# Performance work log

Hardware: AMD Instinct MI355X
Metric: run time of the kernel (lower is better)

The kernel has to match this reference:

```python
import jax, jax.numpy as jnp
import numpy as np

N, E, D = 100_000, 1_250_000, 64
EPS = 1e-8

def setup_inputs() -> dict:
    key = jax.random.key(0)
    ks = jax.random.split(key, 8)
    h = jax.random.normal(ks[0], (N, D), jnp.float32)
    eig = jax.random.normal(ks[1], (E, 1), jnp.float32)          # per-edge vector field
    snorm_n = jax.random.uniform(ks[2], (N, 1), jnp.float32)     # node norm
    src = jax.random.randint(ks[3], (E,), 0, N)
    dst = jax.random.randint(ks[4], (E,), 0, N)
    # pretrans: Linear(2D -> D); posttrans: Linear((3+1)*D -> D); torch Linear weight is [out, in]
    W1 = jax.random.normal(ks[5], (D, 2 * D), jnp.float32) / np.sqrt(2.0 * D)
    b1 = jnp.zeros((D,), jnp.float32)
    W2 = jax.random.normal(ks[6], (D, 4 * D), jnp.float32) / np.sqrt(4.0 * D)
    b2 = jnp.zeros((D,), jnp.float32)
    gamma = jnp.ones((D,), jnp.float32)   # BatchNorm1d weight
    beta = jnp.zeros((D,), jnp.float32)   # BatchNorm1d bias
    return dict(h=h, eig=eig, snorm_n=snorm_n, src=src, dst=dst,
                W1=W1, b1=b1, W2=W2, b2=b2, gamma=gamma, beta=beta)

def reference(h, eig, snorm_n, src, dst, W1, b1, W2, b2, gamma, beta):
    seg = lambda x: jax.ops.segment_sum(x, dst, num_segments=N)
    # pretrans on edges: MLP(cat[h_src, h_dst])
    z2 = jnp.concatenate([h[src], h[dst]], axis=1)   # [E, 2D]
    e = z2 @ W1.T + b1                                # [E, D]
    deg = seg(jnp.ones((E, 1), e.dtype))              # [N, 1]
    # aggregator: mean
    agg_mean = seg(e) / jnp.maximum(deg, 1.0)
    # aggregator: max (empty segments -> 0)
    agg_max = jax.ops.segment_max(e, dst, num_segments=N)
    agg_max = jnp.where(deg > 0, agg_max, 0.0)
    # aggregator: directional derivative dir_dx
    absum = seg(jnp.abs(eig))                         # [N, 1] sum of |vf| per node
    w = eig / (absum[dst] + EPS)                      # [E, 1] normalized weights
    agg_dir = jnp.abs(seg(e * w) - seg(w) * h)        # [N, D]
    # posttrans on nodes
    hc = jnp.concatenate([h, agg_mean, agg_max, agg_dir], axis=1)  # [N, 4D]
    h2 = (hc @ W2.T + b2) * snorm_n
    # BatchNorm1d (training mode: batch stats, biased variance)
    mu = jnp.mean(h2, axis=0)
    var = jnp.var(h2, axis=0)
    h2 = (h2 - mu) * jax.lax.rsqrt(var + 1e-5) * gamma + beta
    h2 = jax.nn.relu(h2)
    # residual (in_dim == out_dim); dropout p=0 is identity
    return h + h2
```

## Files before the change

kernel.cpp:

```cpp
#include <hip/hip_runtime.h>
#include <math.h>

__device__ __forceinline__ float bf2f(unsigned short s) {
    return __uint_as_float(((unsigned)s) << 16);
}
__device__ __forceinline__ unsigned short f2bf(float f) {
    unsigned u = __float_as_uint(f);
    unsigned r = (u + 0x7fffu + ((u >> 16) & 1u)) >> 16;
    return (unsigned short)r;
}

__global__ __launch_bounds__(256) void edge_rank_kernel(
    const int* __restrict__ dst, int* __restrict__ cursor, int* __restrict__ rank, int E)
{
    int e = blockIdx.x * 256 + threadIdx.x;
    if (e < E) {
        rank[e] = atomicAdd(&cursor[dst[e]], 1);
    }
}

__global__ __launch_bounds__(256) void block_reduce_kernel(
    const int* __restrict__ deg, int* __restrict__ bsum, int N)
{
    __shared__ int sd[256];
    int t = threadIdx.x;
    int i = blockIdx.x * 256 + t;
    sd[t] = (i < N) ? deg[i] : 0;
    __syncthreads();
    for (int s = 128; s > 0; s >>= 1) {
        if (t < s) sd[t] += sd[t + s];
        __syncthreads();
    }
    if (t == 0) bsum[blockIdx.x] = sd[0];
}

__global__ __launch_bounds__(1024) void scan_bsums_kernel(
    const int* __restrict__ bsum, int* __restrict__ bscan, int nb)
{
    __shared__ int sd[1024];
    int t = threadIdx.x;
    int own = (t < nb) ? bsum[t] : 0;
    sd[t] = own;
    __syncthreads();
    for (int off = 1; off < 1024; off <<= 1) {
        int v = (t >= off) ? sd[t - off] : 0;
        __syncthreads();
        sd[t] += v;
        __syncthreads();
    }
    if (t < nb) bscan[t] = sd[t] - own;
}

__global__ __launch_bounds__(256) void block_scan_kernel(
    const int* __restrict__ deg, const int* __restrict__ bscan,
    int* __restrict__ offs, int N)
{
    __shared__ int sd[256];
    int t = threadIdx.x;
    int i = blockIdx.x * 256 + t;
    int myv = (i < N) ? deg[i] : 0;
    sd[t] = myv;
    __syncthreads();
    for (int off = 1; off < 256; off <<= 1) {
        int v = (t >= off) ? sd[t - off] : 0;
        __syncthreads();
        sd[t] += v;
        __syncthreads();
    }
    if (i < N) {
        offs[i] = sd[t] - myv + bscan[blockIdx.x];
    }
}

__global__ __launch_bounds__(256) void csr_scatter_kernel(
    const int* __restrict__ src, const int* __restrict__ dst, const float* __restrict__ eig,
    const int* __restrict__ rank, const int* __restrict__ offs,
    int2* __restrict__ csr, int E)
{
    int e = blockIdx.x * 256 + threadIdx.x;
    if (e < E) {
        int dn = dst[e];
        int p = offs[dn] + rank[e];
        csr[p] = make_int2(src[e], __float_as_int(eig[e]));
    }
}

__global__ __launch_bounds__(256) void uv_kernel(
    const float* __restrict__ h, const float* __restrict__ W1, const float* __restrict__ b1,
    unsigned short* __restrict__ u, unsigned short* __restrict__ v, int N)
{
    __shared__ float wT[64 * 128];
    __shared__ float hs[64 * 68];
    int t = threadIdx.x;
    for (int idx = t; idx < 64 * 128; idx += 256) {
        int j = idx >> 7, c = idx & 127;
        int d = c & 63;
        int col = (c < 64) ? j : (64 + j);
        wT[idx] = W1[d * 128 + col];
    }
    int n0 = blockIdx.x * 64;
    for (int r = 0; r < 16; ++r) {
        int idx = r * 256 + t;
        int nl = idx >> 6, j = idx & 63;
        int n = n0 + nl;
        hs[nl * 68 + j] = (n < N) ? h[(size_t)n * 64 + j] : 0.f;
    }
    __syncthreads();

    int nb = (t & 15) * 4;
    int cb = (t >> 4) * 8;
    float acc[4][8];
#pragma unroll
    for (int i = 0; i < 4; ++i)
#pragma unroll
        for (int k = 0; k < 8; ++k) acc[i][k] = 0.f;

    for (int j = 0; j < 64; ++j) {
        float wv[8];
#pragma unroll
        for (int k = 0; k < 8; ++k) wv[k] = wT[j * 128 + cb + k];
#pragma unroll
        for (int i = 0; i < 4; ++i) {
            float hv = hs[(nb + i) * 68 + j];
#pragma unroll
            for (int k = 0; k < 8; ++k) acc[i][k] = fmaf(hv, wv[k], acc[i][k]);
        }
    }

    bool isV = (cb >= 64);
    int dbase = cb & 63;
#pragma unroll
    for (int i = 0; i < 4; ++i) {
        int n = n0 + nb + i;
        if (n < N) {
            union { unsigned short s[8]; uint4 v4; } pk;
            if (!isV) {
#pragma unroll
                for (int k = 0; k < 8; ++k) pk.s[k] = f2bf(acc[i][k]);
                *(uint4*)(u + (size_t)n * 64 + dbase) = pk.v4;
            } else {
#pragma unroll
                for (int k = 0; k < 8; ++k) pk.s[k] = f2bf(acc[i][k] + b1[dbase + k]);
                *(uint4*)(v + (size_t)n * 64 + dbase) = pk.v4;
            }
        }
    }
}

__global__ __launch_bounds__(256) void w2t_kernel(
    const float* __restrict__ W2, float* __restrict__ w2t)
{
    int idx = blockIdx.x * 256 + threadIdx.x;
    if (idx < 64 * 256) {
        int d = idx >> 8, k = idx & 255;
        w2t[k * 64 + d] = W2[idx];
    }
}

__global__ __launch_bounds__(256) void agg_kernel(
    const unsigned short* __restrict__ u, const unsigned short* __restrict__ v,
    const float* __restrict__ h,
    const int* __restrict__ offs, const int* __restrict__ degi,
    const int2* __restrict__ csr,
    unsigned short* __restrict__ agg, int N)
{
    int gw = (blockIdx.x * 256 + threadIdx.x) >> 6;
    int lane = threadIdx.x & 63;
    int n = __builtin_amdgcn_readfirstlane(gw);
    if (n >= N) return;
    int beg = offs[n];
    int dn = degi[n];

    float accs = 0.f, accd = 0.f, accm = -3.402823466e38f;
    float pa = 0.f, ps = 0.f;
    for (int i0 = 0; i0 < dn; i0 += 64) {
        int cnt = min(dn - i0, 64);
        int idxv = 0; float wvv = 0.f;
        if (lane < cnt) {
            int2 rec = csr[beg + i0 + lane];
            idxv = rec.x;
            wvv = __int_as_float(rec.y);
        }
        pa += fabsf(wvv);
        ps += wvv;
        int j = 0;
        for (; j + 4 <= cnt; j += 4) {
            int s0 = __shfl(idxv, j), s1 = __shfl(idxv, j + 1);
            int s2 = __shfl(idxv, j + 2), s3 = __shfl(idxv, j + 3);
            float w0 = __shfl(wvv, j), w1 = __shfl(wvv, j + 1);
            float w2_ = __shfl(wvv, j + 2), w3 = __shfl(wvv, j + 3);
            float u0 = bf2f(u[(size_t)s0 * 64 + lane]);
            float u1 = bf2f(u[(size_t)s1 * 64 + lane]);
            float u2 = bf2f(u[(size_t)s2 * 64 + lane]);
            float u3 = bf2f(u[(size_t)s3 * 64 + lane]);
            accs += (u0 + u1) + (u2 + u3);
            accm = fmaxf(accm, fmaxf(fmaxf(u0, u1), fmaxf(u2, u3)));
            accd = fmaf(w0, u0, fmaf(w1, u1, fmaf(w2_, u2, fmaf(w3, u3, accd))));
        }
        for (; j < cnt; ++j) {
            int s0 = __shfl(idxv, j);
            float w0 = __shfl(wvv, j);
            float u0 = bf2f(u[(size_t)s0 * 64 + lane]);
            accs += u0;
            accm = fmaxf(accm, u0);
            accd = fmaf(w0, u0, accd);
        }
    }
#pragma unroll
    for (int w = 1; w < 64; w <<= 1) {
        pa += __shfl_xor(pa, w);
        ps += __shfl_xor(ps, w);
    }
    float inv_ab = 1.f / (pa + 1e-8f);
    float segw = ps * inv_ab;

    float vl = bf2f(v[(size_t)n * 64 + lane]);
    float hl = h[(size_t)n * 64 + lane];
    float fdeg = (float)dn;
    float mean = (accs + fdeg * vl) / fmaxf(fdeg, 1.f);
    float amax = (dn > 0) ? (accm + vl) : 0.f;
    float adir = fabsf(fmaf(accd, inv_ab, segw * (vl - hl)));
    size_t base = (size_t)n * 192;
    agg[base + lane]       = f2bf(mean);
    agg[base + 64 + lane]  = f2bf(amax);
    agg[base + 128 + lane] = f2bf(adir);
}

__global__ __launch_bounds__(256) void post_gemm_kernel(
    const float* __restrict__ h, const unsigned short* __restrict__ agg,
    const float* __restrict__ w2t, const float* __restrict__ b2,
    const float* __restrict__ snorm, float* __restrict__ h2,
    float* __restrict__ bn_buf, int N)
{
    __shared__ float hcS[64 * 65];
    int tid = threadIdx.x;
    int node = tid & 63;
    int q = __builtin_amdgcn_readfirstlane(tid >> 6);
    int n0 = blockIdx.x * 64;
    int n = n0 + node;
    float acc[16];
#pragma unroll
    for (int i = 0; i < 16; ++i) acc[i] = 0.f;

    for (int c = 0; c < 4; ++c) {
        if (c == 0) {
            for (int it = 0; it < 4; ++it) {
                int idx = it * 256 + tid;
                int r = idx >> 4, c4 = idx & 15;
                int nn = n0 + r;
                float4 val = make_float4(0.f, 0.f, 0.f, 0.f);
                if (nn < N) val = *(const float4*)(h + (size_t)nn * 64 + c4 * 4);
                int kk = c4 * 4;
                hcS[(kk + 0) * 65 + r] = val.x;
                hcS[(kk + 1) * 65 + r] = val.y;
                hcS[(kk + 2) * 65 + r] = val.z;
                hcS[(kk + 3) * 65 + r] = val.w;
            }
        } else {
            for (int it = 0; it < 2; ++it) {
                int idx = it * 256 + tid;
                int r = idx >> 3, j8 = idx & 7;
                int nn = n0 + r;
                uint4 val = make_uint4(0, 0, 0, 0);
                if (nn < N) val = *(const uint4*)(agg + (size_t)nn * 192 + (c - 1) * 64 + j8 * 8);
                unsigned short* ps = (unsigned short*)&val;
                int kk = j8 * 8;
#pragma unroll
                for (int m = 0; m < 8; ++m)
                    hcS[(kk + m) * 65 + r] = bf2f(ps[m]);
            }
        }
        __syncthreads();
        const float* wbase = w2t + c * 64 * 64 + q * 16;
        for (int k = 0; k < 64; ++k) {
            float hv = hcS[k * 65 + node];
            const float* wr = wbase + k * 64;
#pragma unroll
            for (int i = 0; i < 16; ++i)
                acc[i] = fmaf(wr[i], hv, acc[i]);
        }
        __syncthreads();
    }

    float sn = (n < N) ? snorm[n] : 0.f;
#pragma unroll
    for (int i = 0; i < 16; ++i) acc[i] = (acc[i] + b2[q * 16 + i]) * sn;

    if (n < N) {
#pragma unroll
        for (int i = 0; i < 4; ++i) {
            float4 o = make_float4(acc[i * 4], acc[i * 4 + 1], acc[i * 4 + 2], acc[i * 4 + 3]);
            *(float4*)(h2 + (size_t)n * 64 + q * 16 + i * 4) = o;
        }
    }

#pragma unroll
    for (int i = 0; i < 16; ++i) hcS[(q * 16 + i) * 65 + node] = acc[i];
    __syncthreads();
    if (tid < 64) {
        float s1 = 0.f, s2 = 0.f;
        for (int r = 0; r < 64; ++r) {
            float x = hcS[tid * 65 + r];
            s1 += x;
            s2 = fmaf(x, x, s2);
        }
        atomicAdd(&bn_buf[tid], s1);
        atomicAdd(&bn_buf[64 + tid], s2);
    }
}

__global__ __launch_bounds__(256) void bn_final_kernel(
    const float* __restrict__ h, const float* __restrict__ h2,
    const float* __restrict__ bn_buf, const float* __restrict__ gamma,
    const float* __restrict__ beta, float* __restrict__ out, int N, float invN)
{
    int idx = blockIdx.x * 256 + threadIdx.x;
    int total4 = N * 16;
    if (idx >= total4) return;
    int base = idx * 4;
    int d0 = base & 63;
    const float4 a = *(const float4*)(h2 + base);
    const float4 hh = *(const float4*)(h + base);
    float r[4] = {a.x, a.y, a.z, a.w};
    float hv[4] = {hh.x, hh.y, hh.z, hh.w};
    float o[4];
#pragma unroll
    for (int k = 0; k < 4; ++k) {
        int d = d0 + k;
        float mu = bn_buf[d] * invN;
        float var = bn_buf[64 + d] * invN - mu * mu;
        float rstd = rsqrtf(var + 1e-5f);
        float x = (r[k] - mu) * rstd * gamma[d] + beta[d];
        o[k] = hv[k] + fmaxf(x, 0.f);
    }
    float4 ov = {o[0], o[1], o[2], o[3]};
    *(float4*)(out + base) = ov;
}

extern "C" void kernel_launch(void* const* d_in, const int* in_sizes, int n_in,
                              void* d_out, int out_size, void* d_ws, size_t ws_size,
                              hipStream_t stream)
{
    const float* h     = (const float*)d_in[0];
    const float* eig   = (const float*)d_in[1];
    const float* snorm = (const float*)d_in[2];
    const int*   src   = (const int*)d_in[3];
    const int*   dst   = (const int*)d_in[4];
    const float* W1    = (const float*)d_in[5];
    const float* b1    = (const float*)d_in[6];
    const float* W2    = (const float*)d_in[7];
    const float* b2    = (const float*)d_in[8];
    const float* gamma = (const float*)d_in[9];
    const float* beta  = (const float*)d_in[10];
    float* out = (float*)d_out;

    const int N = in_sizes[2];
    const int E = in_sizes[1];

    char* w = (char*)d_ws;
    size_t off = 0;
    auto alloc = [&](size_t bytes) -> char* {
        char* p = w + off;
        off += (bytes + 255) & ~size_t(255);
        return p;
    };
    unsigned short* u = (unsigned short*)alloc((size_t)N * 64 * 2);
    unsigned short* v = (unsigned short*)alloc((size_t)N * 64 * 2);
    float* h2 = (float*)u;
    unsigned short* agg = (unsigned short*)alloc((size_t)N * 192 * 2);
    int2* csr = (int2*)alloc((size_t)E * 8);
    int*  rank = (int*)alloc((size_t)E * 4);
    char* zero_base = w + off;
    int*   cursor = (int*)alloc((size_t)N * 4);
    float* bn_buf = (float*)alloc(128 * 4);
    size_t zero_bytes = (size_t)((char*)(bn_buf + 128) - zero_base);
    int* offs = (int*)alloc((size_t)N * 4);
    int nb = (N + 255) / 256;
    int* bsum  = (int*)alloc((size_t)nb * 4);
    int* bscan = (int*)alloc((size_t)nb * 4);
    float* w2t = (float*)alloc(64 * 256 * 4);
    (void)ws_size; (void)n_in; (void)out_size;

    hipMemsetAsync(zero_base, 0, zero_bytes, stream);

    int egrid = (E + 255) / 256;
    edge_rank_kernel<<<egrid, 256, 0, stream>>>(dst, cursor, rank, E);
    block_reduce_kernel<<<nb, 256, 0, stream>>>(cursor, bsum, N);
    scan_bsums_kernel<<<1, 1024, 0, stream>>>(bsum, bscan, nb);
    block_scan_kernel<<<nb, 256, 0, stream>>>(cursor, bscan, offs, N);
    csr_scatter_kernel<<<egrid, 256, 0, stream>>>(src, dst, eig, rank, offs, csr, E);

    int ntiles = (N + 63) / 64;
    uv_kernel<<<ntiles, 256, 0, stream>>>(h, W1, b1, u, v, N);
    w2t_kernel<<<64, 256, 0, stream>>>(W2, w2t);

    int agrid = ((size_t)N * 64 + 255) / 256;
    agg_kernel<<<agrid, 256, 0, stream>>>(u, v, h, offs, cursor, csr, agg, N);

    post_gemm_kernel<<<(N + 63) / 64, 256, 0, stream>>>(h, agg, w2t, b2, snorm,
                                                        h2, bn_buf, N);

    int fgrid = (N * 16 + 255) / 256;
    bn_final_kernel<<<fgrid, 256, 0, stream>>>(h, h2, bn_buf, gamma, beta, out, N, 1.0f / (float)N);
}
```

Before: 389.7 us.

## Replace scalar post-GEMM with bf16 MFMA reading a packed bf16 hc buffer

The agg kernel now writes h (converted to bf16) together with mean, max and dir into one 256-wide bf16 row per node. A new post kernel computes the posttrans GEMM with 16x16x32 bf16 MFMA instructions, loading operands straight from global memory with no LDS staging. W2 is converted to bf16 instead of being transposed. Batch-norm partial sums are reduced with shuffles before the atomics. This targets the FP32 FMA and LDS cost of the old GEMM, but rounding h to bf16 inside the GEMM adds precision loss. Padded rows (Npad) are read uninitialised, though they are masked on output.

```diff
diff --git a/kernel.cpp b/kernel.cpp
--- a/kernel.cpp
+++ b/kernel.cpp
@@ -1,5 +1,8 @@
 #include <hip/hip_runtime.h>
 #include <math.h>
+
+typedef __attribute__((ext_vector_type(8))) short bf16x8;
+typedef __attribute__((ext_vector_type(4))) float f32x4;
 
 __device__ __forceinline__ float bf2f(unsigned short s) {
     return __uint_as_float(((unsigned)s) << 16);
@@ -147,14 +150,11 @@
     }
 }
 
-__global__ __launch_bounds__(256) void w2t_kernel(
-    const float* __restrict__ W2, float* __restrict__ w2t)
+__global__ __launch_bounds__(256) void w2b_kernel(
+    const float* __restrict__ W2, unsigned short* __restrict__ w2b)
 {
     int idx = blockIdx.x * 256 + threadIdx.x;
-    if (idx < 64 * 256) {
-        int d = idx >> 8, k = idx & 255;
-        w2t[k * 64 + d] = W2[idx];
-    }
+    if (idx < 64 * 256) w2b[idx] = f2bf(W2[idx]);
 }
 
 __global__ __launch_bounds__(256) void agg_kernel(
@@ -162,7 +162,7 @@
     const float* __restrict__ h,
     const int* __restrict__ offs, const int* __restrict__ degi,
     const int2* __restrict__ csr,
-    unsigned short* __restrict__ agg, int N)
+    unsigned short* __restrict__ hc, int N)
 {
     int gw = (blockIdx.x * 256 + threadIdx.x) >> 6;
     int lane = threadIdx.x & 63;
@@ -220,92 +220,82 @@
     float mean = (accs + fdeg * vl) / fmaxf(fdeg, 1.f);
     float amax = (dn > 0) ? (accm + vl) : 0.f;
     float adir = fabsf(fmaf(accd, inv_ab, segw * (vl - hl)));
-    size_t base = (size_t)n * 192;
-    agg[base + lane]       = f2bf(mean);
-    agg[base + 64 + lane]  = f2bf(amax);
-    agg[base + 128 + lane] = f2bf(adir);
-}
-
-__global__ __launch_bounds__(256) void post_gemm_kernel(
-    const float* __restrict__ h, const unsigned short* __restrict__ agg,
-    const float* __restrict__ w2t, const float* __restrict__ b2,
-    const float* __restrict__ snorm, float* __restrict__ h2,
-    float* __restrict__ bn_buf, int N)
-{
-    __shared__ float hcS[64 * 65];
+    size_t base = (size_t)n * 256;
+    hc[base + lane]       = f2bf(hl);
+    hc[base + 64 + lane]  = f2bf(mean);
+    hc[base + 128 + lane] = f2bf(amax);
+    hc[base + 192 + lane] = f2bf(adir);
+}
+
+__global__ __launch_bounds__(256) void post_mfma_kernel(
+    const unsigned short* __restrict__ hc, const unsigned short* __restrict__ w2b,
+    const float* __restrict__ b2, const float* __restrict__ snorm,
+    float* __restrict__ h2, float* __restrict__ bn_buf, int N)
+{
     int tid = threadIdx.x;
-    int node = tid & 63;
-    int q = __builtin_amdgcn_readfirstlane(tid >> 6);
+    int lane = tid & 63;
+    int wv = tid >> 6;
+    int l15 = lane & 15;
+    int quad = lane >> 4;
     int n0 = blockIdx.x * 64;
-    int n = n0 + node;
-    float acc[16];
-#pragma unroll
-    for (int i = 0; i < 16; ++i) acc[i] = 0.f;
-
+    int m0 = n0 + wv * 16;
+
+    const unsigned short* aptr = hc + (size_t)(m0 + l15) * 256 + quad * 8;
+    const unsigned short* bptr = w2b + (size_t)l15 * 256 + quad * 8;
+
+    f32x4 acc[4];
+#pragma unroll
+    for (int c = 0; c < 4; ++c) acc[c] = (f32x4){0.f, 0.f, 0.f, 0.f};
+
+#pragma unroll
+    for (int ks = 0; ks < 8; ++ks) {
+        bf16x8 a = *(const bf16x8*)(aptr + ks * 32);
+#pragma unroll
+        for (int c = 0; c < 4; ++c) {
+            bf16x8 b = *(const bf16x8*)(bptr + (size_t)c * 16 * 256 + ks * 32);
+            acc[c] = __builtin_amdgcn_mfma_f32_16x16x32_bf16(a, b, acc[c], 0, 0, 0);
+        }
+    }
+
+    float sn[4];
+    int nodes[4];
+#pragma unroll
+    for (int r = 0; r < 4; ++r) {
+        nodes[r] = m0 + quad * 4 + r;
+        sn[r] = (nodes[r] < N) ? snorm[nodes[r]] : 0.f;
+    }
+    float s1[4], s2[4];
+#pragma unroll
+    for (int c = 0; c < 4; ++c) { s1[c] = 0.f; s2[c] = 0.f; }
+
+#pragma unroll
     for (int c = 0; c < 4; ++c) {
-        if (c == 0) {
-            for (int it = 0; it < 4; ++it) {
-                int idx = it * 256 + tid;
-                int r = idx >> 4, c4 = idx & 15;
-                int nn = n0 + r;
-                float4 val = make_float4(0.f, 0.f, 0.f, 0.f);
-                if (nn < N) val = *(const float4*)(h + (size_t)nn * 64 + c4 * 4);
-                int kk = c4 * 4;
-                hcS[(kk + 0) * 65 + r] = val.x;
-                hcS[(kk + 1) * 65 + r] = val.y;
-                hcS[(kk + 2) * 65 + r] = val.z;
-                hcS[(kk + 3) * 65 + r] = val.w;
+        int d = c * 16 + l15;
+        float bias = b2[d];
+#pragma unroll
+        for (int r = 0; r < 4; ++r) {
+            float val = (acc[c][r] + bias) * sn[r];
+            if (nodes[r] < N) {
+                h2[(size_t)nodes[r] * 64 + d] = val;
+                s1[c] += val;
+                s2[c] = fmaf(val, val, s2[c]);
             }
-        } else {
-            for (int it = 0; it < 2; ++it) {
-                int idx = it * 256 + tid;
-                int r = idx >> 3, j8 = idx & 7;
-                int nn = n0 + r;
-                uint4 val = make_uint4(0, 0, 0, 0);
-                if (nn < N) val = *(const uint4*)(agg + (size_t)nn * 192 + (c - 1) * 64 + j8 * 8);
-                unsigned short* ps = (unsigned short*)&val;
-                int kk = j8 * 8;
-#pragma unroll
-                for (int m = 0; m < 8; ++m)
-                    hcS[(kk + m) * 65 + r] = bf2f(ps[m]);
-            }
-        }
-        __syncthreads();
-        const float* wbase = w2t + c * 64 * 64 + q * 16;
-        for (int k = 0; k < 64; ++k) {
-            float hv = hcS[k * 65 + node];
-            const float* wr = wbase + k * 64;
-#pragma unroll
-            for (int i = 0; i < 16; ++i)
-                acc[i] = fmaf(wr[i], hv, acc[i]);
-        }
-        __syncthreads();
-    }
-
-    float sn = (n < N) ? snorm[n] : 0.f;
-#pragma unroll
-    for (int i = 0; i < 16; ++i) acc[i] = (acc[i] + b2[q * 16 + i]) * sn;
-
-    if (n < N) {
-#pragma unroll
-        for (int i = 0; i < 4; ++i) {
-            float4 o = make_float4(acc[i * 4], acc[i * 4 + 1], acc[i * 4 + 2], acc[i * 4 + 3]);
-            *(float4*)(h2 + (size_t)n * 64 + q * 16 + i * 4) = o;
-        }
-    }
-
-#pragma unroll
-    for (int i = 0; i < 16; ++i) hcS[(q * 16 + i) * 65 + node] = acc[i];
-    __syncthreads();
-    if (tid < 64) {
-        float s1 = 0.f, s2 = 0.f;
-        for (int r = 0; r < 64; ++r) {
-            float x = hcS[tid * 65 + r];
-            s1 += x;
-            s2 = fmaf(x, x, s2);
-        }
-        atomicAdd(&bn_buf[tid], s1);
-        atomicAdd(&bn_buf[64 + tid], s2);
+        }
+    }
+#pragma unroll
+    for (int c = 0; c < 4; ++c) {
+        s1[c] += __shfl_xor(s1[c], 16);
+        s1[c] += __shfl_xor(s1[c], 32);
+        s2[c] += __shfl_xor(s2[c], 16);
+        s2[c] += __shfl_xor(s2[c], 32);
+    }
+    if (lane < 16) {
+#pragma unroll
+        for (int c = 0; c < 4; ++c) {
+            int d = c * 16 + l15;
+            atomicAdd(&bn_buf[d], s1[c]);
+            atomicAdd(&bn_buf[64 + d], s2[c]);
+        }
     }
 }
 
@@ -356,6 +346,7 @@
 
     const int N = in_sizes[2];
     const int E = in_sizes[1];
+    const int Npad = (N + 63) & ~63;
 
     char* w = (char*)d_ws;
     size_t off = 0;
@@ -367,7 +358,7 @@
     unsigned short* u = (unsigned short*)alloc((size_t)N * 64 * 2);
     unsigned short* v = (unsigned short*)alloc((size_t)N * 64 * 2);
     float* h2 = (float*)u;
-    unsigned short* agg = (unsigned short*)alloc((size_t)N * 192 * 2);
+    unsigned short* hc = (unsigned short*)alloc((size_t)Npad * 256 * 2);
     int2* csr = (int2*)alloc((size_t)E * 8);
     int*  rank = (int*)alloc((size_t)E * 4);
     char* zero_base = w + off;
@@ -378,7 +369,7 @@
     int nb = (N + 255) / 256;
     int* bsum  = (int*)alloc((size_t)nb * 4);
     int* bscan = (int*)alloc((size_t)nb * 4);
-    float* w2t = (float*)alloc(64 * 256 * 4);
+    unsigned short* w2b = (unsigned short*)alloc(64 * 256 * 2);
     (void)ws_size; (void)n_in; (void)out_size;
 
     hipMemsetAsync(zero_base, 0, zero_bytes, stream);
@@ -392,13 +383,12 @@
 
     int ntiles = (N + 63) / 64;
     uv_kernel<<<ntiles, 256, 0, stream>>>(h, W1, b1, u, v, N);
-    w2t_kernel<<<64, 256, 0, stream>>>(W2, w2t);
+    w2b_kernel<<<64, 256, 0, stream>>>(W2, w2b);
 
     int agrid = ((size_t)N * 64 + 255) / 256;
-    agg_kernel<<<agrid, 256, 0, stream>>>(u, v, h, offs, cursor, csr, agg, N);
-
-    post_gemm_kernel<<<(N + 63) / 64, 256, 0, stream>>>(h, agg, w2t, b2, snorm,
-                                                        h2, bn_buf, N);
+    agg_kernel<<<agrid, 256, 0, stream>>>(u, v, h, offs, cursor, csr, hc, N);
+
+    post_mfma_kernel<<<Npad / 64, 256, 0, stream>>>(hc, w2b, b2, snorm, h2, bn_buf, N);
 
     int fgrid = (N * 16 + 255) / 256;
     bn_final_kernel<<<fgrid, 256, 0, stream>>>(h, h2, bn_buf, gamma, beta, out, N, 1.0f / (float)N);
```

Result: slower. 492.1 us (+26.3%).
